# Performance work log

Hardware: AMD Instinct MI355X
Metric: run time of the kernel (lower is better)

The kernel has to match this reference:

```python
import jax, jax.numpy as jnp
import numpy as np

B, N, D, DEPTH = 1, 512, 128, 4


def mlp_apply(W, x):
    # W: (depth, d, d), x: (..., d). First layer has no activation, then silu before each matmul.
    x = x @ W[0]
    for i in range(1, DEPTH):
        x = jax.nn.silu(x) @ W[i]
    return x


def _binop(x, y):
    # linear recurrence combine: s_t = a_t * s_{t-1} + b_t
    a1, b1 = x
    a2, b2 = y
    return (a1 * a2, a2 * b1 + b2)


def setup_inputs() -> dict:
    key = jax.random.key(0)
    ks = jax.random.split(key, 7)
    s = 0.02  # scale for projection weights (torch Linear-like init magnitude)
    return {
        "seq": jax.random.normal(ks[0], (B, N, D), jnp.float32),
        "W_mem": jax.random.normal(ks[1], (DEPTH, D, D), jnp.float32) * (D ** -0.5),
        "W_q": jax.random.normal(ks[2], (D, D), jnp.float32) * s,
        "W_kv": jax.random.normal(ks[3], (D, 2 * D), jnp.float32) * s,
        "W_mom": jax.random.normal(ks[4], (D, 1), jnp.float32) * s,
        "W_step": jax.random.normal(ks[5], (D, 1), jnp.float32) * s,
        "W_decay": jax.random.normal(ks[6], (D, 1), jnp.float32) * s,
    }


def reference(seq, W_mem, W_q, W_kv, W_mom, W_step, W_decay):
    b, n, d = seq.shape
    # --- store_memories ---
    adaptive_lr = (seq @ W_step)[..., 0]            # (b, n)
    adaptive_mom = seq @ W_mom                      # (b, n, 1)
    decay = jax.nn.sigmoid(seq @ W_decay)           # (b, n, 1)

    kv = seq.reshape(b * n, d) @ W_kv               # (bn, 2d)
    keys, values = kv[:, :d], kv[:, d:]

    def loss_fn(W, k, v):
        pred = mlp_apply(W, k)                      # (d,)
        # (pred - v)^2 .mean(-1).sum() for a single sample == mean over d
        return jnp.mean((pred - v) ** 2)

    # per-sample meta-gradients wrt memory MLP weights
    losses, grads = jax.vmap(jax.value_and_grad(loss_fn, argnums=0), in_axes=(None, 0, 0))(W_mem, keys, values)
    grads = grads.reshape(b, n, DEPTH, d, d)
    surprise = grads * (-adaptive_lr)[..., None, None, None]   # (b,n,depth,d,d)

    # momentum_t = adaptive_mom_t * momentum_{t-1} + surprise_t  (assoc. scan over n)
    am = adaptive_mom[..., None, None]              # (b, n, 1, 1, 1)
    _, momentum = jax.lax.associative_scan(_binop, (am, surprise), axis=1)

    # update_t = (1 - decay_t) * update_{t-1} + momentum_t
    dec = (1.0 - decay)[..., None, None]            # (b, n, 1, 1, 1)
    _, updates = jax.lax.associative_scan(_binop, (dec, momentum), axis=1)

    # --- retrieve_memories with per-token updated weights ---
    q = (seq @ W_q).reshape(b * n, d)
    W_tok = (W_mem[None, None] + updates).reshape(b * n, DEPTH, d, d)
    retrieved = jax.vmap(mlp_apply)(W_tok, q).reshape(b, n, d)
    return retrieved
```

## Files before the change

### kernel.cpp

```cpp
#include <hip/hip_runtime.h>
#include <hip/hip_bf16.h>
#include <math.h>

#define N 512
#define D 128
#define DD (D*D)
#define ND (N*D)

__device__ __forceinline__ float sigmoidf_(float x) { return 1.f / (1.f + expf(-x)); }

__global__ void k_transpose(const float* __restrict__ W_mem, float* __restrict__ WT) {
    int idx = blockIdx.x * 256 + threadIdx.x;
    int l = idx / DD;
    int r = idx % DD;
    int i = r / D;
    int j = r % D;
    WT[idx] = W_mem[(l + 1) * DD + j * D + i];
}

__global__ __launch_bounds__(512) void k_phase1(
    const float* __restrict__ seq, const float* __restrict__ W_mem,
    const float* __restrict__ W_q, const float* __restrict__ W_kv,
    const float* __restrict__ W_mom, const float* __restrict__ W_step,
    const float* __restrict__ W_decay, const float* __restrict__ WT,
    float* __restrict__ Q, float* __restrict__ INS, float* __restrict__ ES,
    float* __restrict__ am, float* __restrict__ dec)
{
    __shared__ float s_seq[D], s_v[D], s_cur[D];
    __shared__ float s_h[4][D];
    __shared__ float s_part[4][D];
    __shared__ float s_p3[4][3][D];
    __shared__ float s_red[8];
    __shared__ float s_lr;

    const int t = blockIdx.x;
    const int tid = threadIdx.x;
    const int j = tid & 127;
    const int p = tid >> 7;
    const int i0 = p * 32;

    if (p == 0) s_seq[j] = seq[t * D + j];
    __syncthreads();

    float ps = 0.f;
    if (p == 1) ps = s_seq[j] * W_step[j];
    else if (p == 2) ps = s_seq[j] * W_mom[j];
    else if (p == 3) ps = s_seq[j] * W_decay[j];
#pragma unroll
    for (int off = 32; off > 0; off >>= 1) ps += __shfl_down(ps, off);
    if ((tid & 63) == 0) s_red[tid >> 6] = ps;
    __syncthreads();
    if (tid == 0) s_lr = s_red[2] + s_red[3];
    else if (tid == 1) am[t] = s_red[4] + s_red[5];
    else if (tid == 2) dec[t] = 1.f - sigmoidf_(s_red[6] + s_red[7]);

    float kp = 0.f, vp = 0.f, qp = 0.f;
#pragma unroll 8
    for (int ii = 0; ii < 32; ii++) {
        int i = i0 + ii;
        float si = s_seq[i];
        kp += si * W_kv[i * 256 + j];
        vp += si * W_kv[i * 256 + 128 + j];
        qp += si * W_q[i * 128 + j];
    }
    s_p3[p][0][j] = kp; s_p3[p][1][j] = vp; s_p3[p][2][j] = qp;
    __syncthreads();
    if (p == 0) {
        float kj = s_p3[0][0][j] + s_p3[1][0][j] + s_p3[2][0][j] + s_p3[3][0][j];
        s_cur[j] = kj;
        INS[t * D + j] = kj;
    } else if (p == 1) {
        s_v[j] = s_p3[0][1][j] + s_p3[1][1][j] + s_p3[2][1][j] + s_p3[3][1][j];
    } else if (p == 2) {
        Q[t * D + j] = s_p3[0][2][j] + s_p3[1][2][j] + s_p3[2][2][j] + s_p3[3][2][j];
    }
    __syncthreads();

    for (int l = 0; l < 4; l++) {
        const float* Wl = W_mem + l * DD;
        float yp = 0.f;
#pragma unroll 8
        for (int ii = 0; ii < 32; ii++) {
            int i = i0 + ii;
            yp += s_cur[i] * Wl[i * D + j];
        }
        s_part[p][j] = yp;
        __syncthreads();
        if (p == 0) {
            float y = s_part[0][j] + s_part[1][j] + s_part[2][j] + s_part[3][j];
            s_h[l][j] = y;
            if (l < 3) {
                float a = y * sigmoidf_(y);
                s_cur[j] = a;
                INS[(l + 1) * ND + t * D + j] = a;
            }
        }
        __syncthreads();
    }

    if (p == 0) {
        float e = -s_lr * (2.f / (float)D) * (s_h[3][j] - s_v[j]);
        ES[3 * ND + t * D + j] = e;
        s_cur[j] = e;
    }
    __syncthreads();

    for (int l = 3; l >= 1; l--) {
        const float* Wt = WT + (l - 1) * DD;
        float gp = 0.f;
#pragma unroll 8
        for (int ii = 0; ii < 32; ii++) {
            int i = i0 + ii;
            gp += s_cur[i] * Wt[i * D + j];
        }
        s_part[p][j] = gp;
        __syncthreads();
        if (p == 0) {
            float g = s_part[0][j] + s_part[1][j] + s_part[2][j] + s_part[3][j];
            float h = s_h[l - 1][j];
            float sg = sigmoidf_(h);
            float e2 = g * (sg * (1.f + h * (1.f - sg)));
            ES[(l - 1) * ND + t * D + j] = e2;
            s_cur[j] = e2;
        }
        __syncthreads();
    }
}

__global__ __launch_bounds__(512) void k_logscan(
    const float* __restrict__ am, const float* __restrict__ dec,
    double* __restrict__ LA, double* __restrict__ LDp, int* __restrict__ NC)
{
    __shared__ double sa[N], sd[N];
    __shared__ int sn[N];
    const int t = threadIdx.x;
    float a = am[t];
    float d = dec[t];
    sa[t] = log((double)fmaxf(fabsf(a), 1e-38f));
    sd[t] = log((double)fmaxf(d, 1e-38f));
    sn[t] = (a < 0.f) ? 1 : 0;
    __syncthreads();
    for (int off = 1; off < N; off <<= 1) {
        double va = 0.0, vd = 0.0; int vn = 0;
        if (t >= off) { va = sa[t - off]; vd = sd[t - off]; vn = sn[t - off]; }
        __syncthreads();
        sa[t] += va; sd[t] += vd; sn[t] += vn;
        __syncthreads();
    }
    LA[t] = sa[t]; LDp[t] = sd[t]; NC[t] = sn[t];
}

__global__ __launch_bounds__(256) void k_build(
    const double* __restrict__ LA, const double* __restrict__ LDp,
    const int* __restrict__ NC,
    float* __restrict__ Amat, float* __restrict__ Dmat)
{
    int idx = blockIdx.x * 256 + threadIdx.x;
    int u = idx >> 9;
    int s = idx & (N - 1);
    float va = 0.f, vd = 0.f;
    if (s <= u) {
        va = expf((float)(LA[u] - LA[s]));
        if ((NC[u] - NC[s]) & 1) va = -va;
        vd = expf((float)(LDp[u] - LDp[s]));
    }
    Amat[idx] = va;
    Dmat[idx] = vd;
}

__global__ __launch_bounds__(256) void k_betamm(
    const float* __restrict__ Dmat, const float* __restrict__ Amat,
    float* __restrict__ beta)
{
    const int bs = blockIdx.x;
    const int bt = blockIdx.y;
    const int z  = blockIdx.z;
    if (bs > bt) return;
    const int span = bt - bs + 1;
    const int chunk = (span + 3) >> 2;
    const int kBeg = bs + z * chunk;
    const int kEnd = (kBeg + chunk < bt + 1) ? (kBeg + chunk) : (bt + 1);
    if (kBeg >= kEnd) return;

    __shared__ float sD[32][33];
    __shared__ float sA[32][33];

    const int tx = threadIdx.x & 31;
    const int ty = threadIdx.x >> 5;
    float acc[4] = {0.f, 0.f, 0.f, 0.f};

    for (int kt = kBeg; kt < kEnd; kt++) {
        for (int i = threadIdx.x; i < 1024; i += 256) {
            int r = i >> 5, c = i & 31;
            sD[r][c] = Dmat[(bt * 32 + r) * N + kt * 32 + c];
            sA[r][c] = Amat[(kt * 32 + r) * N + bs * 32 + c];
        }
        __syncthreads();
#pragma unroll 8
        for (int k = 0; k < 32; k++) {
            float a = sA[k][tx];
#pragma unroll
            for (int j = 0; j < 4; j++)
                acc[j] += sD[ty + 8 * j][k] * a;
        }
        __syncthreads();
    }
#pragma unroll
    for (int j = 0; j < 4; j++)
        atomicAdd(&beta[(bt * 32 + ty + 8 * j) * N + bs * 32 + tx], acc[j]);
}

__global__ __launch_bounds__(512) void k_phase3(
    const float* __restrict__ Q, float* __restrict__ out,
    const float* __restrict__ W_mem, const float* __restrict__ INS,
    const float* __restrict__ ES, const float* __restrict__ beta)
{
    __shared__ float s_x[D];
    __shared__ float s_c[N];
    __shared__ float s_part[4][D];

    const int t = blockIdx.x;
    const int tid = threadIdx.x;
    const int j = tid & 127;
    const int p = tid >> 7;
    const int i0 = p * 32;
    const int cnt = t + 1;
    const int chunk = (cnt + 3) >> 2;
    const int sBeg = p * chunk;
    const int sEnd = (sBeg + chunk < cnt) ? (sBeg + chunk) : cnt;
    const float brow = (tid <= t) ? beta[t * N + tid] : 0.f;

    if (p == 0) s_x[j] = Q[t * D + j];
    __syncthreads();

    for (int l = 0; l < 4; l++) {
        const float* INSl = INS + l * ND;
        const float* ESl  = ES + l * ND;
        const float* Wl   = W_mem + l * DD;

        if (tid <= t) {
            const float4* ip = (const float4*)(INSl + tid * D);
            const float4* xp = (const float4*)s_x;
            float acc = 0.f;
#pragma unroll 8
            for (int i = 0; i < 32; i++) {
                float4 a = xp[i];
                float4 b = ip[i];
                acc += a.x * b.x + a.y * b.y + a.z * b.z + a.w * b.w;
            }
            s_c[tid] = brow * acc;
        }
        __syncthreads();

        float yp = 0.f;
#pragma unroll 4
        for (int s = sBeg; s < sEnd; s++) yp += s_c[s] * ESl[s * D + j];
#pragma unroll 8
        for (int ii = 0; ii < 32; ii++) {
            int i = i0 + ii;
            yp += s_x[i] * Wl[i * D + j];
        }
        s_part[p][j] = yp;
        __syncthreads();

        if (p == 0) {
            float y = s_part[0][j] + s_part[1][j] + s_part[2][j] + s_part[3][j];
            if (l < 3) {
                s_x[j] = y * sigmoidf_(y);
            } else {
                out[t * D + j] = y;
            }
        }
        __syncthreads();
    }
}

extern "C" void kernel_launch(void* const* d_in, const int* in_sizes, int n_in,
                              void* d_out, int out_size, void* d_ws, size_t ws_size,
                              hipStream_t stream) {
    const float* seq     = (const float*)d_in[0];
    const float* W_mem   = (const float*)d_in[1];
    const float* W_q     = (const float*)d_in[2];
    const float* W_kv    = (const float*)d_in[3];
    const float* W_mom   = (const float*)d_in[4];
    const float* W_step  = (const float*)d_in[5];
    const float* W_decay = (const float*)d_in[6];
    float* out = (float*)d_out;

    float* ws   = (float*)d_ws;
    float* am   = ws;
    float* dec  = am + N;
    float* Q    = dec + N;
    float* INS  = Q + ND;
    float* ES   = INS + 4 * ND;
    float* beta = ES + 4 * ND;
    float* X    = beta + N * N;
    float* WT   = X + ND;
    float* Amat = WT + 3 * DD;
    float* Dmat = Amat + N * N;
    double* LA  = (double*)(Dmat + N * N);
    double* LDp = LA + N;
    int* NC     = (int*)(LDp + N);

    hipMemsetAsync(beta, 0, N * N * sizeof(float), stream);
    k_transpose<<<192, 256, 0, stream>>>(W_mem, WT);
    k_phase1<<<N, 512, 0, stream>>>(seq, W_mem, W_q, W_kv, W_mom, W_step, W_decay,
                                    WT, Q, INS, ES, am, dec);
    k_logscan<<<1, N, 0, stream>>>(am, dec, LA, LDp, NC);
    k_build<<<(N * N) / 256, 256, 0, stream>>>(LA, LDp, NC, Amat, Dmat);
    dim3 mmgrid(N / 32, N / 32, 4);
    k_betamm<<<mmgrid, 256, 0, stream>>>(Dmat, Amat, beta);
    k_phase3<<<N, 512, 0, stream>>>(Q, out, W_mem, INS, ES, beta);
}
```

Before: 181.2 us.

## Replace per-token retrieval kernel with tiled per-layer kernels using shared-memory blocks

The single retrieval kernel, which ran one block per token and looped over all four layers, is replaced by four launches of a layer kernel. Each launch tiles 16 tokens against 32-source chunks of the INS/ES factors, plus separate blocks for the dense weight product. Partial results are combined with atomicAdd into zeroed layer buffers, and SiLU is applied when the previous layer's output is loaded. The aim is to reuse INS/ES tiles across many tokens instead of re-reading them per token, at the cost of more launches, extra memsets and atomic traffic.

```diff
diff --git a/kernel.cpp b/kernel.cpp
--- a/kernel.cpp
+++ b/kernel.cpp
@@ -6,6 +6,8 @@
 #define D 128
 #define DD (D*D)
 #define ND (N*D)
+#define LSTR 132
+#define CSTR 36
 
 __device__ __forceinline__ float sigmoidf_(float x) { return 1.f / (1.f + expf(-x)); }
 
@@ -210,68 +212,148 @@
         atomicAdd(&beta[(bt * 32 + ty + 8 * j) * N + bs * 32 + tx], acc[j]);
 }
 
-__global__ __launch_bounds__(512) void k_phase3(
-    const float* __restrict__ Q, float* __restrict__ out,
-    const float* __restrict__ W_mem, const float* __restrict__ INS,
-    const float* __restrict__ ES, const float* __restrict__ beta)
+__global__ __launch_bounds__(64) void k_layer(
+    const float* __restrict__ Xin, float* __restrict__ Yout,
+    const float* __restrict__ Wl, const float* __restrict__ INSl,
+    const float* __restrict__ ESl, const float* __restrict__ beta,
+    int actIn)
 {
-    __shared__ float s_x[D];
-    __shared__ float s_c[N];
-    __shared__ float s_part[4][D];
-
-    const int t = blockIdx.x;
-    const int tid = threadIdx.x;
-    const int j = tid & 127;
-    const int p = tid >> 7;
-    const int i0 = p * 32;
-    const int cnt = t + 1;
-    const int chunk = (cnt + 3) >> 2;
-    const int sBeg = p * chunk;
-    const int sEnd = (sBeg + chunk < cnt) ? (sBeg + chunk) : cnt;
-    const float brow = (tid <= t) ? beta[t * N + tid] : 0.f;
-
-    if (p == 0) s_x[j] = Q[t * D + j];
-    __syncthreads();
-
-    for (int l = 0; l < 4; l++) {
-        const float* INSl = INS + l * ND;
-        const float* ESl  = ES + l * ND;
-        const float* Wl   = W_mem + l * DD;
-
-        if (tid <= t) {
-            const float4* ip = (const float4*)(INSl + tid * D);
-            const float4* xp = (const float4*)s_x;
-            float acc = 0.f;
-#pragma unroll 8
-            for (int i = 0; i < 32; i++) {
-                float4 a = xp[i];
-                float4 b = ip[i];
-                acc += a.x * b.x + a.y * b.y + a.z * b.z + a.w * b.w;
+    const int r = blockIdx.x;
+    const int z = blockIdx.y;
+    const int t0 = r * 16;
+    const int lane = threadIdx.x;
+    const bool isW = (z >= 17);
+    if (!isW && z > (r >> 1)) return;
+
+    __shared__ float sX[16 * LSTR];
+    __shared__ float sI[32 * LSTR];
+    __shared__ float sE[32 * LSTR];
+    __shared__ float sc[16 * CSTR];
+
+#pragma unroll
+    for (int i = 0; i < 8; i++) {
+        int f4 = lane + 64 * i;
+        int row = f4 >> 5, c4 = f4 & 31;
+        float4 v = ((const float4*)(Xin + t0 * D))[f4];
+        if (actIn) {
+            v.x = v.x * sigmoidf_(v.x); v.y = v.y * sigmoidf_(v.y);
+            v.z = v.z * sigmoidf_(v.z); v.w = v.w * sigmoidf_(v.w);
+        }
+        *(float4*)(sX + row * LSTR + c4 * 4) = v;
+    }
+
+    if (isW) {
+        __syncthreads();
+        const int k0 = (z - 17) * 64;
+        const int ti0 = (lane >> 4) * 4;
+        const int jA = (lane & 15) * 4;
+        float acc[4][8];
+#pragma unroll
+        for (int a = 0; a < 4; a++)
+#pragma unroll
+            for (int b = 0; b < 8; b++) acc[a][b] = 0.f;
+
+#pragma unroll 4
+        for (int k = k0; k < k0 + 64; k++) {
+            float4 w0 = *(const float4*)(Wl + k * D + jA);
+            float4 w1 = *(const float4*)(Wl + k * D + 64 + jA);
+            float xv[4];
+#pragma unroll
+            for (int a = 0; a < 4; a++) xv[a] = sX[(ti0 + a) * LSTR + k];
+#pragma unroll
+            for (int a = 0; a < 4; a++) {
+                acc[a][0] += xv[a] * w0.x; acc[a][1] += xv[a] * w0.y;
+                acc[a][2] += xv[a] * w0.z; acc[a][3] += xv[a] * w0.w;
+                acc[a][4] += xv[a] * w1.x; acc[a][5] += xv[a] * w1.y;
+                acc[a][6] += xv[a] * w1.z; acc[a][7] += xv[a] * w1.w;
             }
-            s_c[tid] = brow * acc;
-        }
-        __syncthreads();
-
-        float yp = 0.f;
-#pragma unroll 4
-        for (int s = sBeg; s < sEnd; s++) yp += s_c[s] * ESl[s * D + j];
-#pragma unroll 8
-        for (int ii = 0; ii < 32; ii++) {
-            int i = i0 + ii;
-            yp += s_x[i] * Wl[i * D + j];
-        }
-        s_part[p][j] = yp;
-        __syncthreads();
-
-        if (p == 0) {
-            float y = s_part[0][j] + s_part[1][j] + s_part[2][j] + s_part[3][j];
-            if (l < 3) {
-                s_x[j] = y * sigmoidf_(y);
-            } else {
-                out[t * D + j] = y;
+        }
+#pragma unroll
+        for (int a = 0; a < 4; a++) {
+            float* yp = Yout + (t0 + ti0 + a) * D;
+#pragma unroll
+            for (int q = 0; q < 4; q++) {
+                atomicAdd(yp + jA + q,      acc[a][q]);
+                atomicAdd(yp + 64 + jA + q, acc[a][4 + q]);
             }
         }
-        __syncthreads();
+        return;
+    }
+
+    const int s0 = z * 32;
+#pragma unroll
+    for (int i = 0; i < 16; i++) {
+        int f4 = lane + 64 * i;
+        int row = f4 >> 5, c4 = f4 & 31;
+        float4 a = ((const float4*)(INSl + s0 * D))[f4];
+        float4 b = ((const float4*)(ESl + s0 * D))[f4];
+        *(float4*)(sI + row * LSTR + c4 * 4) = a;
+        *(float4*)(sE + row * LSTR + c4 * 4) = b;
+    }
+    __syncthreads();
+
+    const int tiA = (lane >> 3) * 2;
+    const int siA = lane & 7;
+    float g1[2][4];
+#pragma unroll
+    for (int v = 0; v < 2; v++)
+#pragma unroll
+        for (int u = 0; u < 4; u++) g1[v][u] = 0.f;
+
+    for (int k4 = 0; k4 < D; k4 += 4) {
+        float4 a0 = *(float4*)(sX + tiA * LSTR + k4);
+        float4 a1 = *(float4*)(sX + (tiA + 1) * LSTR + k4);
+#pragma unroll
+        for (int u = 0; u < 4; u++) {
+            float4 b = *(float4*)(sI + (siA + 8 * u) * LSTR + k4);
+            g1[0][u] += a0.x * b.x + a0.y * b.y + a0.z * b.z + a0.w * b.w;
+            g1[1][u] += a1.x * b.x + a1.y * b.y + a1.z * b.z + a1.w * b.w;
+        }
+    }
+#pragma unroll
+    for (int v = 0; v < 2; v++)
+#pragma unroll
+        for (int u = 0; u < 4; u++) {
+            int ti = tiA + v, si = siA + 8 * u;
+            sc[ti * CSTR + si] = g1[v][u] * beta[(t0 + ti) * N + s0 + si];
+        }
+    __syncthreads();
+
+    const int ti0 = (lane >> 4) * 4;
+    const int jA = (lane & 15) * 4;
+    float acc[4][8];
+#pragma unroll
+    for (int a = 0; a < 4; a++)
+#pragma unroll
+        for (int b = 0; b < 8; b++) acc[a][b] = 0.f;
+
+    for (int s4 = 0; s4 < 32; s4 += 4) {
+        float cva[4][4];
+#pragma unroll
+        for (int a = 0; a < 4; a++)
+            *(float4*)cva[a] = *(float4*)(sc + (ti0 + a) * CSTR + s4);
+#pragma unroll
+        for (int u = 0; u < 4; u++) {
+            float4 e0 = *(float4*)(sE + (s4 + u) * LSTR + jA);
+            float4 e1 = *(float4*)(sE + (s4 + u) * LSTR + 64 + jA);
+#pragma unroll
+            for (int a = 0; a < 4; a++) {
+                float cu = cva[a][u];
+                acc[a][0] += cu * e0.x; acc[a][1] += cu * e0.y;
+                acc[a][2] += cu * e0.z; acc[a][3] += cu * e0.w;
+                acc[a][4] += cu * e1.x; acc[a][5] += cu * e1.y;
+                acc[a][6] += cu * e1.z; acc[a][7] += cu * e1.w;
+            }
+        }
+    }
+#pragma unroll
+    for (int a = 0; a < 4; a++) {
+        float* yp = Yout + (t0 + ti0 + a) * D;
+#pragma unroll
+        for (int q = 0; q < 4; q++) {
+            atomicAdd(yp + jA + q,      acc[a][q]);
+            atomicAdd(yp + 64 + jA + q, acc[a][4 + q]);
+        }
     }
 }
 
@@ -294,15 +376,17 @@
     float* INS  = Q + ND;
     float* ES   = INS + 4 * ND;
     float* beta = ES + 4 * ND;
-    float* X    = beta + N * N;
-    float* WT   = X + ND;
+    float* Y012 = beta + N * N;
+    float* WT   = Y012 + 3 * ND;
     float* Amat = WT + 3 * DD;
     float* Dmat = Amat + N * N;
     double* LA  = (double*)(Dmat + N * N);
     double* LDp = LA + N;
     int* NC     = (int*)(LDp + N);
 
-    hipMemsetAsync(beta, 0, N * N * sizeof(float), stream);
+    hipMemsetAsync(beta, 0, (N * N + 3 * ND) * sizeof(float), stream);
+    hipMemsetAsync(out, 0, ND * sizeof(float), stream);
+
     k_transpose<<<192, 256, 0, stream>>>(W_mem, WT);
     k_phase1<<<N, 512, 0, stream>>>(seq, W_mem, W_q, W_kv, W_mom, W_step, W_decay,
                                     WT, Q, INS, ES, am, dec);
@@ -310,5 +394,13 @@
     k_build<<<(N * N) / 256, 256, 0, stream>>>(LA, LDp, NC, Amat, Dmat);
     dim3 mmgrid(N / 32, N / 32, 4);
     k_betamm<<<mmgrid, 256, 0, stream>>>(Dmat, Amat, beta);
-    k_phase3<<<N, 512, 0, stream>>>(Q, out, W_mem, INS, ES, beta);
-}
+
+    float* Y0 = Y012;
+    float* Y1 = Y012 + ND;
+    float* Y2 = Y012 + 2 * ND;
+    dim3 lgrid(32, 19);
+    k_layer<<<lgrid, 64, 0, stream>>>(Q,  Y0,  W_mem,          INS,          ES,          beta, 0);
+    k_layer<<<lgrid, 64, 0, stream>>>(Y0, Y1,  W_mem + DD,     INS + ND,     ES + ND,     beta, 1);
+    k_layer<<<lgrid, 64, 0, stream>>>(Y1, Y2,  W_mem + 2 * DD, INS + 2 * ND, ES + 2 * ND, beta, 1);
+    k_layer<<<lgrid, 64, 0, stream>>>(Y2, out, W_mem + 3 * DD, INS + 3 * ND, ES + 3 * ND, beta, 1);
+}
```

Measured after the change: 186.3 us. +2.8%, slower.
